# Performance work log

Hardware: AMD Instinct MI355X
Metric: run time of the kernel (lower is better)

Reference implementation:

```python
import jax, jax.numpy as jnp
import numpy as np

N = 100000
E = 1600000
F_IN, HID, CLS = 512, 128, 64


def gcn_conv(x, W, b, src, dst, n_nodes):
    """out = D^{-1/2} (A + I) D^{-1/2} (x W) + b, with edge-list (src->dst)."""
    h = x @ W  # [N, D]
    loop = jnp.arange(n_nodes, dtype=src.dtype)
    s = jnp.concatenate([src, loop])  # add self-loops
    d = jnp.concatenate([dst, loop])
    ones = jnp.ones(s.shape[0], dtype=h.dtype)
    deg = jax.ops.segment_sum(ones, d, num_segments=n_nodes)  # >=1 via self-loops
    inv_sqrt = jax.lax.rsqrt(deg)
    coef = inv_sqrt[s] * inv_sqrt[d]  # [E+N]
    msg = h[s] * coef[:, None]  # gather + scale
    out = jax.ops.segment_sum(msg, d, num_segments=n_nodes)
    return out + b


def setup_inputs() -> dict:
    key = jax.random.key(0)
    k = jax.random.split(key, 6)
    x = jax.random.normal(k[0], (N, F_IN), dtype=jnp.float32)
    src = jax.random.randint(k[1], (E,), 0, N, dtype=jnp.int64)
    dst = jax.random.randint(k[2], (E,), 0, N, dtype=jnp.int64)
    W1 = jax.random.normal(k[3], (F_IN, HID), dtype=jnp.float32) / np.sqrt(F_IN)
    b1 = jnp.zeros((HID,), dtype=jnp.float32)
    W2 = jax.random.normal(k[4], (HID, CLS), dtype=jnp.float32) / np.sqrt(HID)
    b2 = jnp.zeros((CLS,), dtype=jnp.float32)
    return {"x": x, "src": src, "dst": dst, "W1": W1, "b1": b1, "W2": W2, "b2": b2}


def reference(x, src, dst, W1, b1, W2, b2):
    h = gcn_conv(x, W1, b1, src, dst, N)
    h = jax.nn.relu(h)
    # dropout is identity in eval mode (training=False)
    h = gcn_conv(h, W2, b2, src, dst, N)
    return jax.nn.log_softmax(h, axis=1)
```

## Files before the change

kernel.cpp:

```cpp
#include <hip/hip_runtime.h>


#define NN 100000
#define EE 1600000
#define F_IN 512
#define HID 128
#define CLS 64
#define CAP 64
#define NBUCK 391
#define EPB 4096
#define EPT 16
#define NBLK 391

typedef __bf16 v8bf __attribute__((ext_vector_type(8)));
typedef float v4f __attribute__((ext_vector_type(4)));
typedef unsigned int uint;
typedef unsigned short ushort;

__device__ __forceinline__ float bf_lo(uint u) { return __uint_as_float(u << 16); }
__device__ __forceinline__ float bf_hi(uint u) { return __uint_as_float(u & 0xffff0000u); }


__global__ void cvt_weights(const float* __restrict__ W1, const float* __restrict__ W2,
                            __bf16* __restrict__ W1t, __bf16* __restrict__ W2t) {
    int i = blockIdx.x * 256 + threadIdx.x;
    if (i < F_IN * HID) { int k = i / HID, n = i % HID; W1t[(size_t)n * F_IN + k] = (__bf16)W1[i]; }
    if (i < HID * CLS)  { int k = i / CLS,  n = i % CLS; W2t[(size_t)n * HID + k] = (__bf16)W2[i]; }
}

template<int BM, int BN, int BK, int K>
__global__ __launch_bounds__(256) void fused_bin_gemm1(
        const float* __restrict__ X, const __bf16* __restrict__ Bt,
        __bf16* __restrict__ Out, int M,
        const int* __restrict__ src, const int* __restrict__ dst,
        int* __restrict__ boff, int* __restrict__ bcnt, uint* __restrict__ bbuf) {
    constexpr int SA = BK + 8;
    constexpr int SB = BK + 8;
    constexpr int LDS_BYTES = (BM * SA + BN * SB) * 2;
    static_assert(EPB * 4 + (NBUCK + 1) * 8 + 49 * 4 <= LDS_BYTES, "build LDS fits");
    __shared__ __align__(16) char smem[LDS_BYTES];
    const int tid = threadIdx.x;

    if (blockIdx.x < NBLK) {
        uint* lrec  = (uint*)smem;
        int*  lhist = (int*)(smem + EPB * 4);
        int*  loff  = lhist + (NBUCK + 1);
        int*  asum  = loff + (NBUCK + 1);
        const int blk = blockIdx.x;
        const int base = blk * EPB;
        for (int i = tid; i < NBUCK + 1; i += 256) lhist[i] = 0;
        __syncthreads();
        uint rec[EPT]; int bk[EPT], pos[EPT];
        #pragma unroll
        for (int j = 0; j < EPT; ++j) {
            int idx = base + tid + j * 256;
            bool ok = idx < EE;
            int ii = ok ? idx : 0;
            unsigned ud = (unsigned)dst[ii]; if (ud >= NN) ud = 0;
            unsigned us = (unsigned)src[ii]; if (us >= NN) us = 0;
            rec[j] = (us << 8) | (ud & 255u);
            bk[j] = ok ? (int)(ud >> 8) : NBUCK;
            pos[j] = atomicAdd(&lhist[bk[j]], 1);
        }
        __syncthreads();
        if (tid < 49) {
            int s = 0;
            #pragma unroll
            for (int k = 0; k < 8; ++k) s += lhist[tid * 8 + k];
            asum[tid] = s;
        }
        __syncthreads();
        if (tid == 0) {
            int run = 0;
            for (int g = 0; g < 49; ++g) { int t = asum[g]; asum[g] = run; run += t; }
        }
        __syncthreads();
        if (tid < 49) {
            int run = asum[tid];
            #pragma unroll
            for (int k = 0; k < 8; ++k) { loff[tid * 8 + k] = run; run += lhist[tid * 8 + k]; }
        }
        __syncthreads();
        #pragma unroll
        for (int j = 0; j < EPT; ++j)
            lrec[loff[bk[j]] + pos[j]] = rec[j];
        __syncthreads();
        for (int i = tid; i < EPB; i += 256)
            bbuf[base + i] = lrec[i];
        for (int q = tid; q < NBUCK; q += 256) {
            boff[q * NBLK + blk] = base + loff[q];
            bcnt[q * NBLK + blk] = lhist[q];
        }
        return;
    }

    __bf16* As = (__bf16*)smem;
    __bf16* Bs = As + BM * SA;
    const int m0 = (blockIdx.x - NBLK) * BM;
    constexpr int WM = BM / 2, WN = BN / 2;
    constexpr int MT = WM / 16, NT = WN / 16;
    const int w = tid >> 6, lane = tid & 63;
    const int wm = w & 1, wn = w >> 1;
    const int lr = lane & 15;
    const int lq = lane >> 4;

    v4f acc[MT][NT] = {};

    for (int k0 = 0; k0 < K; k0 += BK) {
        {
            constexpr int CH = BM * (BK / 8);
            for (int sgi = tid; sgi < CH; sgi += 256) {
                int row = sgi / (BK / 8), c8 = sgi % (BK / 8);
                int gr = m0 + row; if (gr >= M) gr = M - 1;
                const float* g = X + (size_t)gr * K + k0 + c8 * 8;
                float4 v0 = *(const float4*)g;
                float4 v1 = *(const float4*)(g + 4);
                __bf16 b[8];
                b[0] = (__bf16)v0.x; b[1] = (__bf16)v0.y; b[2] = (__bf16)v0.z; b[3] = (__bf16)v0.w;
                b[4] = (__bf16)v1.x; b[5] = (__bf16)v1.y; b[6] = (__bf16)v1.z; b[7] = (__bf16)v1.w;
                *(uint4*)&As[row * SA + c8 * 8] = *(uint4*)b;
            }
        }
        {
            constexpr int CH = BN * (BK / 8);
            for (int sgi = tid; sgi < CH; sgi += 256) {
                int n = sgi / (BK / 8), c8 = sgi % (BK / 8);
                uint4 val = *(const uint4*)(Bt + (size_t)n * K + k0 + c8 * 8);
                *(uint4*)&Bs[n * SB + c8 * 8] = val;
            }
        }
        __syncthreads();
        #pragma unroll
        for (int kk = 0; kk < BK; kk += 32) {
            v8bf a[MT], bfr[NT];
            #pragma unroll
            for (int i = 0; i < MT; ++i)
                a[i] = *(const v8bf*)&As[(wm * WM + i * 16 + lr) * SA + kk + lq * 8];
            #pragma unroll
            for (int j = 0; j < NT; ++j)
                bfr[j] = *(const v8bf*)&Bs[(wn * WN + j * 16 + lr) * SB + kk + lq * 8];
            #pragma unroll
            for (int i = 0; i < MT; ++i)
                #pragma unroll
                for (int j = 0; j < NT; ++j)
                    acc[i][j] = __builtin_amdgcn_mfma_f32_16x16x32_bf16(a[i], bfr[j], acc[i][j], 0, 0, 0);
        }
        __syncthreads();
    }
    #pragma unroll
    for (int i = 0; i < MT; ++i)
        #pragma unroll
        for (int j = 0; j < NT; ++j)
            #pragma unroll
            for (int r = 0; r < 4; ++r) {
                int row = m0 + wm * WM + i * 16 + lq * 4 + r;
                if (row < M) {
                    int col = wn * WN + j * 16 + lr;
                    Out[(size_t)row * BN + col] = (__bf16)acc[i][j][r];
                }
            }
}

__global__ __launch_bounds__(256) void build_rows(const uint* __restrict__ bbuf,
                                                  const int* __restrict__ boff,
                                                  const int* __restrict__ bcnt,
                                                  int* __restrict__ cnt,
                                                  float* __restrict__ inv,
                                                  int* __restrict__ csr_pad) {
    __shared__ int lcnt[256];
    __shared__ int soff[NBLK];
    __shared__ int sc[392];
    __shared__ int spre[392];
    __shared__ int gsum[49];
    const int q = blockIdx.x, tid = threadIdx.x;
    lcnt[tid] = 0;
    for (int b = tid; b < 392; b += 256) sc[b] = (b < NBLK) ? bcnt[q * NBLK + b] : 0;
    for (int b = tid; b < NBLK; b += 256) soff[b] = boff[q * NBLK + b];
    __syncthreads();
    if (tid < 49) {
        int s = 0;
        #pragma unroll
        for (int k = 0; k < 8; ++k) s += sc[tid * 8 + k];
        gsum[tid] = s;
    }
    __syncthreads();
    if (tid == 0) {
        int run = 0;
        for (int g = 0; g < 49; ++g) { int t = gsum[g]; gsum[g] = run; run += t; }
    }
    __syncthreads();
    if (tid < 49) {
        int run = gsum[tid];
        #pragma unroll
        for (int k = 0; k < 8; ++k) { spre[tid * 8 + k] = run; run += sc[tid * 8 + k]; }
    }
    __syncthreads();
    const int total = spre[391] + sc[391];
    const int v0 = q * 256;
    for (int r = tid; r < total; r += 256) {
        int lo = 0, hi = 390;
        while (hi > lo) { int mid = (lo + hi + 1) >> 1; if (spre[mid] <= r) lo = mid; else hi = mid - 1; }
        uint rec = bbuf[soff[lo] + (r - spre[lo])];
        int vl = (int)(rec & 255u);
        int s  = (int)(rec >> 8);
        int p = atomicAdd(&lcnt[vl], 1);
        if (p < CAP) csr_pad[(size_t)(v0 + vl) * CAP + p] = s;
    }
    __syncthreads();
    int v = v0 + tid;
    if (v < NN) {
        cnt[v] = lcnt[tid];
        inv[v] = rsqrtf((float)(lcnt[tid] + 1));
    }
}

template<int BM, int BN, int BK, int K>
__global__ __launch_bounds__(256) void gemm_bt(const __bf16* __restrict__ A,
                                               const __bf16* __restrict__ Bt,
                                               __bf16* __restrict__ Out, int M) {
    constexpr int SA = BK + 8;
    constexpr int SB = BK + 8;
    __shared__ __align__(16) __bf16 As[BM * SA];
    __shared__ __align__(16) __bf16 Bs[BN * SB];
    const int tid = threadIdx.x;
    const int m0 = blockIdx.x * BM;
    constexpr int WM = BM / 2, WN = BN / 2;
    constexpr int MT = WM / 16, NT = WN / 16;
    const int w = tid >> 6, lane = tid & 63;
    const int wm = w & 1, wn = w >> 1;
    const int lr = lane & 15;
    const int lq = lane >> 4;

    v4f acc[MT][NT] = {};

    for (int k0 = 0; k0 < K; k0 += BK) {
        {
            constexpr int CH = BM * (BK / 8);
            for (int s = tid; s < CH; s += 256) {
                int row = s / (BK / 8), c8 = s % (BK / 8);
                int gr = m0 + row; if (gr >= M) gr = M - 1;
                uint4 val = *(const uint4*)(A + (size_t)gr * K + k0 + c8 * 8);
                *(uint4*)&As[row * SA + c8 * 8] = val;
            }
        }
        {
            constexpr int CH = BN * (BK / 8);
            for (int s = tid; s < CH; s += 256) {
                int n = s / (BK / 8), c8 = s % (BK / 8);
                uint4 val = *(const uint4*)(Bt + (size_t)n * K + k0 + c8 * 8);
                *(uint4*)&Bs[n * SB + c8 * 8] = val;
            }
        }
        __syncthreads();
        #pragma unroll
        for (int kk = 0; kk < BK; kk += 32) {
            v8bf a[MT], bfr[NT];
            #pragma unroll
            for (int i = 0; i < MT; ++i)
                a[i] = *(const v8bf*)&As[(wm * WM + i * 16 + lr) * SA + kk + lq * 8];
            #pragma unroll
            for (int j = 0; j < NT; ++j)
                bfr[j] = *(const v8bf*)&Bs[(wn * WN + j * 16 + lr) * SB + kk + lq * 8];
            #pragma unroll
            for (int i = 0; i < MT; ++i)
                #pragma unroll
                for (int j = 0; j < NT; ++j)
                    acc[i][j] = __builtin_amdgcn_mfma_f32_16x16x32_bf16(a[i], bfr[j], acc[i][j], 0, 0, 0);
        }
        __syncthreads();
    }
    #pragma unroll
    for (int i = 0; i < MT; ++i)
        #pragma unroll
        for (int j = 0; j < NT; ++j)
            #pragma unroll
            for (int r = 0; r < 4; ++r) {
                int row = m0 + wm * WM + i * 16 + lq * 4 + r;
                if (row < M) {
                    int col = wn * WN + j * 16 + lr;
                    Out[(size_t)row * BN + col] = (__bf16)acc[i][j][r];
                }
            }
}


__global__ __launch_bounds__(256) void agg_relu_w(const uint* __restrict__ Hin,
                                                  const float* __restrict__ inv,
                                                  const int* __restrict__ cnt,
                                                  const int* __restrict__ csr_pad,
                                                  const float* __restrict__ bias,
                                                  uint* __restrict__ Hout) {
    const int wid = threadIdx.x >> 6, lane = threadIdx.x & 63;
    const int v = blockIdx.x * 4 + wid;
    if (v >= NN) return;
    const float isv = inv[v];
    const int n_e = min(cnt[v], CAP);
    int sidx = 0;
    if (lane < n_e) sidx = csr_pad[(size_t)v * CAP + lane];
    float c = inv[sidx] * isv;
    uint u = Hin[(size_t)v * 64 + lane];
    float ax = bf_lo(u) * isv * isv;
    float ay = bf_hi(u) * isv * isv;
    int j = 0;
    for (; j + 3 < n_e; j += 4) {
        int s0 = __shfl(sidx, j), s1 = __shfl(sidx, j + 1);
        int s2 = __shfl(sidx, j + 2), s3 = __shfl(sidx, j + 3);
        float c0 = __shfl(c, j), c1 = __shfl(c, j + 1);
        float c2 = __shfl(c, j + 2), c3 = __shfl(c, j + 3);
        uint h0 = Hin[(size_t)s0 * 64 + lane];
        uint h1 = Hin[(size_t)s1 * 64 + lane];
        uint h2 = Hin[(size_t)s2 * 64 + lane];
        uint h3 = Hin[(size_t)s3 * 64 + lane];
        ax += c0 * bf_lo(h0); ay += c0 * bf_hi(h0);
        ax += c1 * bf_lo(h1); ay += c1 * bf_hi(h1);
        ax += c2 * bf_lo(h2); ay += c2 * bf_hi(h2);
        ax += c3 * bf_lo(h3); ay += c3 * bf_hi(h3);
    }
    for (; j < n_e; ++j) {
        int s0 = __shfl(sidx, j);
        float c0 = __shfl(c, j);
        uint h0 = Hin[(size_t)s0 * 64 + lane];
        ax += c0 * bf_lo(h0); ay += c0 * bf_hi(h0);
    }
    float ox = fmaxf(ax + bias[2 * lane], 0.f);
    float oy = fmaxf(ay + bias[2 * lane + 1], 0.f);
    __bf16 blo = (__bf16)ox, bhi = (__bf16)oy;
    uint res = (uint)*(ushort*)&blo | ((uint)*(ushort*)&bhi << 16);
    Hout[(size_t)v * 64 + lane] = res;
}

__global__ __launch_bounds__(256) void agg_softmax_w(const ushort* __restrict__ Hin,
                                                     const float* __restrict__ inv,
                                                     const int* __restrict__ cnt,
                                                     const int* __restrict__ csr_pad,
                                                     const float* __restrict__ bias,
                                                     float* __restrict__ out) {
    const int wid = threadIdx.x >> 6, lane = threadIdx.x & 63;
    const int v = blockIdx.x * 4 + wid;
    if (v >= NN) return;
    const float isv = inv[v];
    const int n_e = min(cnt[v], CAP);
    int sidx = 0;
    if (lane < n_e) sidx = csr_pad[(size_t)v * CAP + lane];
    float c = inv[sidx] * isv;
    uint u = (uint)Hin[(size_t)v * 64 + lane];
    float acc = __uint_as_float(u << 16) * isv * isv;
    int j = 0;
    for (; j + 3 < n_e; j += 4) {
        int s0 = __shfl(sidx, j), s1 = __shfl(sidx, j + 1);
        int s2 = __shfl(sidx, j + 2), s3 = __shfl(sidx, j + 3);
        float c0 = __shfl(c, j), c1 = __shfl(c, j + 1);
        float c2 = __shfl(c, j + 2), c3 = __shfl(c, j + 3);
        uint h0 = (uint)Hin[(size_t)s0 * 64 + lane];
        uint h1 = (uint)Hin[(size_t)s1 * 64 + lane];
        uint h2 = (uint)Hin[(size_t)s2 * 64 + lane];
        uint h3 = (uint)Hin[(size_t)s3 * 64 + lane];
        acc += c0 * __uint_as_float(h0 << 16);
        acc += c1 * __uint_as_float(h1 << 16);
        acc += c2 * __uint_as_float(h2 << 16);
        acc += c3 * __uint_as_float(h3 << 16);
    }
    for (; j < n_e; ++j) {
        int s0 = __shfl(sidx, j);
        float c0 = __shfl(c, j);
        uint h0 = (uint)Hin[(size_t)s0 * 64 + lane];
        acc += c0 * __uint_as_float(h0 << 16);
    }
    float o = acc + bias[lane];
    float m = o;
    #pragma unroll
    for (int off = 32; off >= 1; off >>= 1) m = fmaxf(m, __shfl_xor(m, off, 64));
    float e = __expf(o - m);
    float s = e;
    #pragma unroll
    for (int off = 32; off >= 1; off >>= 1) s += __shfl_xor(s, off, 64);
    out[(size_t)v * CLS + lane] = (o - m) - __logf(s);
}


extern "C" void kernel_launch(void* const* d_in, const int* in_sizes, int n_in,
                              void* d_out, int out_size, void* d_ws, size_t ws_size,
                              hipStream_t stream) {
    const float* x   = (const float*)d_in[0];
    const int*   src = (const int*)d_in[1];
    const int*   dst = (const int*)d_in[2];
    const float* W1  = (const float*)d_in[3];
    const float* b1  = (const float*)d_in[4];
    const float* W2  = (const float*)d_in[5];
    const float* b2  = (const float*)d_in[6];
    float* out = (float*)d_out;

    char* p = (char*)d_ws;
    size_t off = 0;
    auto alloc = [&](size_t bytes) {
        off = (off + 255) & ~(size_t)255;
        char* r = p + off;
        off += bytes;
        return r;
    };
    int*    cnt     = (int*)alloc(NN * 4);
    float*  inv     = (float*)alloc(NN * 4);
    int*    boff    = (int*)alloc((size_t)NBUCK * NBLK * 4);
    int*    bcnt    = (int*)alloc((size_t)NBUCK * NBLK * 4);
    uint*   bbuf    = (uint*)alloc((size_t)NBLK * EPB * 4);
    int*    csr_pad = (int*)alloc((size_t)NN * CAP * 4);
    __bf16* W1t     = (__bf16*)alloc((size_t)F_IN * HID * 2);
    __bf16* W2t     = (__bf16*)alloc((size_t)HID * CLS * 2);
    __bf16* P1b     = (__bf16*)alloc((size_t)NN * HID * 2);
    __bf16* H1b     = (__bf16*)alloc((size_t)NN * HID * 2);
    __bf16* P2b     = (__bf16*)alloc((size_t)NN * CLS * 2);

    cvt_weights<<<(F_IN * HID + 255) / 256, 256, 0, stream>>>(W1, W2, W1t, W2t);

    const int MB1 = (NN + 127) / 128;
    fused_bin_gemm1<128, HID, 32, F_IN><<<NBLK + MB1, 256, 0, stream>>>(
        x, W1t, P1b, NN, src, dst, boff, bcnt, bbuf);

    build_rows<<<NBUCK, 256, 0, stream>>>(bbuf, boff, bcnt, cnt, inv, csr_pad);

    agg_relu_w<<<(NN + 3) / 4, 256, 0, stream>>>((const uint*)P1b, inv, cnt, csr_pad, b1, (uint*)H1b);

    gemm_bt<128, CLS, 128, HID><<<MB1, 256, 0, stream>>>(H1b, W2t, P2b, NN);

    agg_softmax_w<<<(NN + 3) / 4, 256, 0, stream>>>((const ushort*)P2b, inv, cnt, csr_pad, b2, out);
}
```

Baseline: 499.4 us.

## Register-prefetch GEMM1 tiles, widen BK, and stage CSR rows in shared memory

The first GEMM now loads the next K-slice of X and W1 into registers while MFMAs run on the current LDS tile, and its K tile grows from 32 to 64. This is meant to hide global load latency and halve the number of barrier iterations. build_rows now scatters each block's padded CSR rows into a 64 KB LDS window and writes them out with coalesced int4 stores instead of scattered global writes. The costs are more registers and LDS, which may lower occupancy, plus padding the csr_pad allocation. The total-count change (spre[391] instead of spre[391]+sc[391]) looks suspicious and may drop the last bucket's records.

```diff
diff --git a/kernel.cpp b/kernel.cpp
--- a/kernel.cpp
+++ b/kernel.cpp
@@ -104,32 +104,56 @@
     const int lr = lane & 15;
     const int lq = lane >> 4;
 
+    constexpr int C8 = BK / 8;
+    constexpr int APT = BM * C8 / 256;
+    constexpr int BPT = BN * C8 / 256;
+
     v4f acc[MT][NT] = {};
-
+    float4 ga[APT][2];
+    uint4  gb[BPT];
+
+    auto prefetch = [&](int k0) {
+        #pragma unroll
+        for (int c = 0; c < APT; ++c) {
+            int sgi = tid + c * 256;
+            int row = sgi / C8, c8 = sgi % C8;
+            int gr = m0 + row; if (gr >= M) gr = M - 1;
+            const float* g = X + (size_t)gr * K + k0 + c8 * 8;
+            ga[c][0] = *(const float4*)g;
+            ga[c][1] = *(const float4*)(g + 4);
+        }
+        #pragma unroll
+        for (int c = 0; c < BPT; ++c) {
+            int sgi = tid + c * 256;
+            int n = sgi / C8, c8 = sgi % C8;
+            gb[c] = *(const uint4*)(Bt + (size_t)n * K + k0 + c8 * 8);
+        }
+    };
+    auto commit = [&]() {
+        #pragma unroll
+        for (int c = 0; c < APT; ++c) {
+            int sgi = tid + c * 256;
+            int row = sgi / C8, c8 = sgi % C8;
+            __bf16 b[8];
+            b[0] = (__bf16)ga[c][0].x; b[1] = (__bf16)ga[c][0].y;
+            b[2] = (__bf16)ga[c][0].z; b[3] = (__bf16)ga[c][0].w;
+            b[4] = (__bf16)ga[c][1].x; b[5] = (__bf16)ga[c][1].y;
+            b[6] = (__bf16)ga[c][1].z; b[7] = (__bf16)ga[c][1].w;
+            *(uint4*)&As[row * SA + c8 * 8] = *(uint4*)b;
+        }
+        #pragma unroll
+        for (int c = 0; c < BPT; ++c) {
+            int sgi = tid + c * 256;
+            int n = sgi / C8, c8 = sgi % C8;
+            *(uint4*)&Bs[n * SB + c8 * 8] = gb[c];
+        }
+    };
+
+    prefetch(0);
     for (int k0 = 0; k0 < K; k0 += BK) {
-        {
-            constexpr int CH = BM * (BK / 8);
-            for (int sgi = tid; sgi < CH; sgi += 256) {
-                int row = sgi / (BK / 8), c8 = sgi % (BK / 8);
-                int gr = m0 + row; if (gr >= M) gr = M - 1;
-                const float* g = X + (size_t)gr * K + k0 + c8 * 8;
-                float4 v0 = *(const float4*)g;
-                float4 v1 = *(const float4*)(g + 4);
-                __bf16 b[8];
-                b[0] = (__bf16)v0.x; b[1] = (__bf16)v0.y; b[2] = (__bf16)v0.z; b[3] = (__bf16)v0.w;
-                b[4] = (__bf16)v1.x; b[5] = (__bf16)v1.y; b[6] = (__bf16)v1.z; b[7] = (__bf16)v1.w;
-                *(uint4*)&As[row * SA + c8 * 8] = *(uint4*)b;
-            }
-        }
-        {
-            constexpr int CH = BN * (BK / 8);
-            for (int sgi = tid; sgi < CH; sgi += 256) {
-                int n = sgi / (BK / 8), c8 = sgi % (BK / 8);
-                uint4 val = *(const uint4*)(Bt + (size_t)n * K + k0 + c8 * 8);
-                *(uint4*)&Bs[n * SB + c8 * 8] = val;
-            }
-        }
-        __syncthreads();
+        commit();
+        __syncthreads();
+        if (k0 + BK < K) prefetch(k0 + BK);
         #pragma unroll
         for (int kk = 0; kk < BK; kk += 32) {
             v8bf a[MT], bfr[NT];
@@ -172,6 +196,7 @@
     __shared__ int sc[392];
     __shared__ int spre[392];
     __shared__ int gsum[49];
+    __shared__ __align__(16) int win[256 * CAP];
     const int q = blockIdx.x, tid = threadIdx.x;
     lcnt[tid] = 0;
     for (int b = tid; b < 392; b += 256) sc[b] = (b < NBLK) ? bcnt[q * NBLK + b] : 0;
@@ -195,7 +220,7 @@
         for (int k = 0; k < 8; ++k) { spre[tid * 8 + k] = run; run += sc[tid * 8 + k]; }
     }
     __syncthreads();
-    const int total = spre[391] + sc[391];
+    const int total = spre[391];
     const int v0 = q * 256;
     for (int r = tid; r < total; r += 256) {
         int lo = 0, hi = 390;
@@ -204,9 +229,14 @@
         int vl = (int)(rec & 255u);
         int s  = (int)(rec >> 8);
         int p = atomicAdd(&lcnt[vl], 1);
-        if (p < CAP) csr_pad[(size_t)(v0 + vl) * CAP + p] = s;
+        if (p < CAP) win[vl * CAP + p] = s;
     }
     __syncthreads();
+    {
+        const int4* s4 = (const int4*)win;
+        int4* d4 = (int4*)(csr_pad + (size_t)v0 * CAP);
+        for (int i = tid; i < 256 * CAP / 4; i += 256) d4[i] = s4[i];
+    }
     int v = v0 + tid;
     if (v < NN) {
         cnt[v] = lcnt[tid];
@@ -403,7 +433,7 @@
     int*    boff    = (int*)alloc((size_t)NBUCK * NBLK * 4);
     int*    bcnt    = (int*)alloc((size_t)NBUCK * NBLK * 4);
     uint*   bbuf    = (uint*)alloc((size_t)NBLK * EPB * 4);
-    int*    csr_pad = (int*)alloc((size_t)NN * CAP * 4);
+    int*    csr_pad = (int*)alloc((size_t)(NN + 256) * CAP * 4);
     __bf16* W1t     = (__bf16*)alloc((size_t)F_IN * HID * 2);
     __bf16* W2t     = (__bf16*)alloc((size_t)HID * CLS * 2);
     __bf16* P1b     = (__bf16*)alloc((size_t)NN * HID * 2);
@@ -413,7 +443,7 @@
     cvt_weights<<<(F_IN * HID + 255) / 256, 256, 0, stream>>>(W1, W2, W1t, W2t);
 
     const int MB1 = (NN + 127) / 128;
-    fused_bin_gemm1<128, HID, 32, F_IN><<<NBLK + MB1, 256, 0, stream>>>(
+    fused_bin_gemm1<128, HID, 64, F_IN><<<NBLK + MB1, 256, 0, stream>>>(
         x, W1t, P1b, NN, src, dst, boff, bcnt, bbuf);
 
     build_rows<<<NBUCK, 256, 0, stream>>>(bbuf, boff, bcnt, cnt, inv, csr_pad);
```

New measurement: 490.3 us. No clear change (-1.8%).

## Use direct global-to-LDS loads in GEMM1 and stage CSR rows in LDS

Applied to the files above, without the earlier changes.

The first GEMM now streams raw fp32 activations and bf16 weights straight into a swizzled LDS layout via global_load_lds, converting to bf16 at fragment-read time, with a larger K tile. The row-building kernel collects each bucket's padded adjacency in LDS and writes it out with coalesced 16-byte stores instead of scattered per-edge global writes. This trades more LDS usage (higher occupancy pressure) and a padded output allocation for fewer register round-trips and better write coalescing.

```diff
diff --git a/kernel.cpp b/kernel.cpp
--- a/kernel.cpp
+++ b/kernel.cpp
@@ -20,6 +20,13 @@
 __device__ __forceinline__ float bf_lo(uint u) { return __uint_as_float(u << 16); }
 __device__ __forceinline__ float bf_hi(uint u) { return __uint_as_float(u & 0xffff0000u); }
 
+__device__ __forceinline__ void load_lds16(const void* g, void* l) {
+    __builtin_amdgcn_global_load_lds(
+        (__attribute__((address_space(1))) void*)(void*)g,
+        (__attribute__((address_space(3))) void*)l,
+        16, 0, 0);
+}
+
 
 __global__ void cvt_weights(const float* __restrict__ W1, const float* __restrict__ W2,
                             __bf16* __restrict__ W1t, __bf16* __restrict__ W2t) {
@@ -34,9 +41,8 @@
         __bf16* __restrict__ Out, int M,
         const int* __restrict__ src, const int* __restrict__ dst,
         int* __restrict__ boff, int* __restrict__ bcnt, uint* __restrict__ bbuf) {
-    constexpr int SA = BK + 8;
-    constexpr int SB = BK + 8;
-    constexpr int LDS_BYTES = (BM * SA + BN * SB) * 2;
+    static_assert(BM == 128 && BN == 128 && BK == 64, "geometry fixed");
+    constexpr int LDS_BYTES = BM * BK * 4 + BN * BK * 2;
     static_assert(EPB * 4 + (NBUCK + 1) * 8 + 49 * 4 <= LDS_BYTES, "build LDS fits");
     __shared__ __align__(16) char smem[LDS_BYTES];
     const int tid = threadIdx.x;
@@ -94,68 +100,72 @@
         return;
     }
 
-    __bf16* As = (__bf16*)smem;
-    __bf16* Bs = As + BM * SA;
+    char* Af = smem;
+    char* Bb = smem + BM * BK * 4;
     const int m0 = (blockIdx.x - NBLK) * BM;
-    constexpr int WM = BM / 2, WN = BN / 2;
-    constexpr int MT = WM / 16, NT = WN / 16;
     const int w = tid >> 6, lane = tid & 63;
     const int wm = w & 1, wn = w >> 1;
     const int lr = lane & 15;
     const int lq = lane >> 4;
 
-    v4f acc[MT][NT] = {};
+    v4f acc[4][4] = {};
 
     for (int k0 = 0; k0 < K; k0 += BK) {
-        {
-            constexpr int CH = BM * (BK / 8);
-            for (int sgi = tid; sgi < CH; sgi += 256) {
-                int row = sgi / (BK / 8), c8 = sgi % (BK / 8);
-                int gr = m0 + row; if (gr >= M) gr = M - 1;
-                const float* g = X + (size_t)gr * K + k0 + c8 * 8;
-                float4 v0 = *(const float4*)g;
-                float4 v1 = *(const float4*)(g + 4);
-                __bf16 b[8];
-                b[0] = (__bf16)v0.x; b[1] = (__bf16)v0.y; b[2] = (__bf16)v0.z; b[3] = (__bf16)v0.w;
-                b[4] = (__bf16)v1.x; b[5] = (__bf16)v1.y; b[6] = (__bf16)v1.z; b[7] = (__bf16)v1.w;
-                *(uint4*)&As[row * SA + c8 * 8] = *(uint4*)b;
-            }
-        }
-        {
-            constexpr int CH = BN * (BK / 8);
-            for (int sgi = tid; sgi < CH; sgi += 256) {
-                int n = sgi / (BK / 8), c8 = sgi % (BK / 8);
-                uint4 val = *(const uint4*)(Bt + (size_t)n * K + k0 + c8 * 8);
-                *(uint4*)&Bs[n * SB + c8 * 8] = val;
-            }
+        #pragma unroll
+        for (int i = 0; i < 8; ++i) {
+            int chunk = w * 8 + i;
+            int r  = chunk * 4 + (lane >> 4);
+            int cb = ((lane & 15) * 16) ^ ((r & 7) << 4);
+            int gr = m0 + r; if (gr >= M) gr = M - 1;
+            load_lds16(X + (size_t)gr * K + k0 + (cb >> 2), Af + chunk * 1024);
+        }
+        #pragma unroll
+        for (int i = 0; i < 4; ++i) {
+            int chunk = w * 4 + i;
+            int n  = chunk * 8 + (lane >> 3);
+            int cb = ((lane & 7) * 16) ^ ((n & 7) << 4);
+            load_lds16(Bt + (size_t)n * K + k0 + (cb >> 1), Bb + chunk * 1024);
         }
         __syncthreads();
         #pragma unroll
         for (int kk = 0; kk < BK; kk += 32) {
-            v8bf a[MT], bfr[NT];
-            #pragma unroll
-            for (int i = 0; i < MT; ++i)
-                a[i] = *(const v8bf*)&As[(wm * WM + i * 16 + lr) * SA + kk + lq * 8];
-            #pragma unroll
-            for (int j = 0; j < NT; ++j)
-                bfr[j] = *(const v8bf*)&Bs[(wn * WN + j * 16 + lr) * SB + kk + lq * 8];
-            #pragma unroll
-            for (int i = 0; i < MT; ++i)
+            v8bf a[4], bfr[4];
+            #pragma unroll
+            for (int i = 0; i < 4; ++i) {
+                int r = wm * 64 + i * 16 + lr;
+                int base = r * 256 + (((kk + lq * 8) * 4) ^ ((r & 7) << 4));
+                float4 f0 = *(const float4*)(Af + base);
+                float4 f1 = *(const float4*)(Af + (base ^ 16));
+                v8bf av;
+                av[0] = (__bf16)f0.x; av[1] = (__bf16)f0.y;
+                av[2] = (__bf16)f0.z; av[3] = (__bf16)f0.w;
+                av[4] = (__bf16)f1.x; av[5] = (__bf16)f1.y;
+                av[6] = (__bf16)f1.z; av[7] = (__bf16)f1.w;
+                a[i] = av;
+            }
+            #pragma unroll
+            for (int j = 0; j < 4; ++j) {
+                int n = wn * 64 + j * 16 + lr;
+                int boff = n * 128 + (((kk + lq * 8) * 2) ^ ((n & 7) << 4));
+                bfr[j] = *(const v8bf*)(Bb + boff);
+            }
+            #pragma unroll
+            for (int i = 0; i < 4; ++i)
                 #pragma unroll
-                for (int j = 0; j < NT; ++j)
+                for (int j = 0; j < 4; ++j)
                     acc[i][j] = __builtin_amdgcn_mfma_f32_16x16x32_bf16(a[i], bfr[j], acc[i][j], 0, 0, 0);
         }
         __syncthreads();
     }
     #pragma unroll
-    for (int i = 0; i < MT; ++i)
-        #pragma unroll
-        for (int j = 0; j < NT; ++j)
+    for (int i = 0; i < 4; ++i)
+        #pragma unroll
+        for (int j = 0; j < 4; ++j)
             #pragma unroll
             for (int r = 0; r < 4; ++r) {
-                int row = m0 + wm * WM + i * 16 + lq * 4 + r;
+                int row = m0 + wm * 64 + i * 16 + lq * 4 + r;
                 if (row < M) {
-                    int col = wn * WN + j * 16 + lr;
+                    int col = wn * 64 + j * 16 + lr;
                     Out[(size_t)row * BN + col] = (__bf16)acc[i][j][r];
                 }
             }
@@ -172,6 +182,7 @@
     __shared__ int sc[392];
     __shared__ int spre[392];
     __shared__ int gsum[49];
+    __shared__ __align__(16) int win[256 * CAP];
     const int q = blockIdx.x, tid = threadIdx.x;
     lcnt[tid] = 0;
     for (int b = tid; b < 392; b += 256) sc[b] = (b < NBLK) ? bcnt[q * NBLK + b] : 0;
@@ -195,7 +206,7 @@
         for (int k = 0; k < 8; ++k) { spre[tid * 8 + k] = run; run += sc[tid * 8 + k]; }
     }
     __syncthreads();
-    const int total = spre[391] + sc[391];
+    const int total = spre[391];
     const int v0 = q * 256;
     for (int r = tid; r < total; r += 256) {
         int lo = 0, hi = 390;
@@ -204,9 +215,14 @@
         int vl = (int)(rec & 255u);
         int s  = (int)(rec >> 8);
         int p = atomicAdd(&lcnt[vl], 1);
-        if (p < CAP) csr_pad[(size_t)(v0 + vl) * CAP + p] = s;
+        if (p < CAP) win[vl * CAP + p] = s;
     }
     __syncthreads();
+    {
+        const int4* s4 = (const int4*)win;
+        int4* d4 = (int4*)(csr_pad + (size_t)v0 * CAP);
+        for (int i = tid; i < 256 * CAP / 4; i += 256) d4[i] = s4[i];
+    }
     int v = v0 + tid;
     if (v < NN) {
         cnt[v] = lcnt[tid];
@@ -403,7 +419,7 @@
     int*    boff    = (int*)alloc((size_t)NBUCK * NBLK * 4);
     int*    bcnt    = (int*)alloc((size_t)NBUCK * NBLK * 4);
     uint*   bbuf    = (uint*)alloc((size_t)NBLK * EPB * 4);
-    int*    csr_pad = (int*)alloc((size_t)NN * CAP * 4);
+    int*    csr_pad = (int*)alloc((size_t)(NN + 256) * CAP * 4);
     __bf16* W1t     = (__bf16*)alloc((size_t)F_IN * HID * 2);
     __bf16* W2t     = (__bf16*)alloc((size_t)HID * CLS * 2);
     __bf16* P1b     = (__bf16*)alloc((size_t)NN * HID * 2);
@@ -413,7 +429,7 @@
     cvt_weights<<<(F_IN * HID + 255) / 256, 256, 0, stream>>>(W1, W2, W1t, W2t);
 
     const int MB1 = (NN + 127) / 128;
-    fused_bin_gemm1<128, HID, 32, F_IN><<<NBLK + MB1, 256, 0, stream>>>(
+    fused_bin_gemm1<128, HID, 64, F_IN><<<NBLK + MB1, 256, 0, stream>>>(
         x, W1t, P1b, NN, src, dst, boff, bcnt, bbuf);
 
     build_rows<<<NBUCK, 256, 0, stream>>>(bbuf, boff, bcnt, cnt, inv, csr_pad);
```

After: 476.7 us. 4.5% less time.
